# Kernel optimization log

Measured on AMD Instinct MI355X. Metric: run time of the kernel, lower is better.

Reference implementation:

```python
import jax, jax.numpy as jnp
import numpy as np

B, FIELDS, D = 4096, 100, 64
HEADS, HID = 4, 16  # concat dim = HEADS*HID = 64


def _pairs(fields):
    # enumerate_fields_fn: all (i, j) with i < j
    left, right = [], []
    for i in range(fields - 1):
        for j in range(i + 1, fields):
            left.append(i)
            right.append(j)
    return np.asarray(left, np.int32), np.asarray(right, np.int32)

LEFT, RIGHT = _pairs(FIELDS)  # each (P,) with P = FIELDS*(FIELDS-1)//2 = 4950


def setup_inputs() -> dict:
    key = jax.random.key(0)
    kx, kq, kk, kv = jax.random.split(key, 4)
    s = 1.0 / np.sqrt(D).astype(np.float32)  # xavier-ish scale
    return {
        "x": jax.random.normal(kx, (B, FIELDS, D), jnp.float32),
        "wq": jax.random.normal(kq, (D, HEADS * HID), jnp.float32) * s,
        "wk": jax.random.normal(kk, (D, HEADS * HID), jnp.float32) * s,
        "wv": jax.random.normal(kv, (D, HEADS * HID), jnp.float32) * s,
    }


def _mha(x, wq, wk, wv):
    # 'origin' multi-head attention: per-head scaled dot product, heads concatenated
    b, f, _ = x.shape
    q = (x @ wq).reshape(b, f, HEADS, HID)
    k = (x @ wk).reshape(b, f, HEADS, HID)
    v = (x @ wv).reshape(b, f, HEADS, HID)
    scores = jnp.einsum('bqhd,bkhd->bhqk', q, k) / jnp.sqrt(jnp.asarray(HID, x.dtype))
    attn = jax.nn.softmax(scores, axis=-1)            # (B, H, F, F)
    z = jnp.einsum('bhqk,bkhd->bqhd', attn, v)        # (B, F, H, HID)
    return z.reshape(b, f, HEADS * HID)


def reference(x, wq, wk, wv):
    # n_layers = 1, product_type = 'inner'
    z = _mha(x, wq, wk, wv)                           # (B, F, 64)
    # torch.gather(z, 1, index=(B,P,1)) -> picks channel 0 only (index shape == output shape)
    z_pol = z[:, LEFT, 0]                             # (B, P)
    x_pol = x[:, RIGHT, 0]                            # (B, P)
    p = z_pol * x_pol                                 # inner product then sum over last dim (size 1)
    # outputs = [sum(p, -1)]; cat along dim 0 of a single layer -> (B, P)
    return p
```

## Files before the change

kernel.cpp:

```cpp
#include <hip/hip_runtime.h>
#include <hip/hip_bf16.h>

namespace {
constexpr int F     = 100;
constexpr int D     = 64;
constexpr int HID   = 16;
constexpr int NPAIR = 4950;
constexpr int NT    = 256;
constexpr int SLD   = 101;
}

__global__ __launch_bounds__(NT, 2) void dcap_kernel(
    const float* __restrict__ x,
    const float* __restrict__ wq,
    const float* __restrict__ wk,
    const float* __restrict__ wv,
    float* __restrict__ out)
{
    __shared__ float sBuf[F * SLD];
    __shared__ float sQT[HID * F];
    __shared__ float sKT[HID * F];
    __shared__ float sWq[D * HID];
    __shared__ float sWk[D * HID];
    __shared__ float sWv[D];
    __shared__ float sV[F];
    __shared__ float sX0[F];
    __shared__ float sZ0[F];

    const int tid = threadIdx.x;
    const int b   = blockIdx.x;
    const float* __restrict__ xb = x + (size_t)b * (F * D);

    for (int i4 = tid; i4 < (F * D) / 4; i4 += NT) {
        const float4 v4 = reinterpret_cast<const float4*>(xb)[i4];
        const int g = i4 * 4;
        const int f = g >> 6;
        const int d = g & 63;
        sBuf[(d + 0) * F + f] = v4.x;
        sBuf[(d + 1) * F + f] = v4.y;
        sBuf[(d + 2) * F + f] = v4.z;
        sBuf[(d + 3) * F + f] = v4.w;
    }
    for (int i = tid; i < D * HID; i += NT) {
        const int d = i >> 4, h = i & 15;
        sWq[i] = wq[d * 64 + h];
        sWk[i] = wk[d * 64 + h];
    }
    if (tid < D) sWv[tid] = wv[tid * 64];
    __syncthreads();

    for (int t = tid; t < 200; t += NT) {
        const int isK = (t >= 100) ? 1 : 0;
        const int tt  = isK ? (t - 100) : t;
        const int f0  = (tt % 25) * 4;
        const int h0  = (tt / 25) * 4;
        const float* __restrict__ W  = isK ? sWk : sWq;
        float* __restrict__       OT = isK ? sKT : sQT;
        float acc[4][4] = {};
        #pragma unroll 8
        for (int d = 0; d < D; ++d) {
            const float4 xv  = *reinterpret_cast<const float4*>(&sBuf[d * F + f0]);
            const float4 wv4 = *reinterpret_cast<const float4*>(&W[d * HID + h0]);
            const float xa[4] = {xv.x, xv.y, xv.z, xv.w};
            const float wa[4] = {wv4.x, wv4.y, wv4.z, wv4.w};
            #pragma unroll
            for (int i = 0; i < 4; ++i)
                #pragma unroll
                for (int j = 0; j < 4; ++j)
                    acc[i][j] = fmaf(xa[i], wa[j], acc[i][j]);
        }
        #pragma unroll
        for (int j = 0; j < 4; ++j)
            #pragma unroll
            for (int i = 0; i < 4; ++i)
                OT[(h0 + j) * F + (f0 + i)] = acc[i][j];
    }
    if (tid < F) {
        float acc = 0.f;
        #pragma unroll 16
        for (int d = 0; d < D; ++d) acc = fmaf(sBuf[d * F + tid], sWv[d], acc);
        sV[tid]  = acc;
        sX0[tid] = sBuf[tid];
    }
    __syncthreads();

    for (int t = tid; t < 625; t += NT) {
        const int q0 = (t / 25) * 4;
        const int k0 = (t % 25) * 4;
        float acc[4][4] = {};
        #pragma unroll
        for (int d = 0; d < HID; ++d) {
            const float4 qv = *reinterpret_cast<const float4*>(&sQT[d * F + q0]);
            const float4 kv = *reinterpret_cast<const float4*>(&sKT[d * F + k0]);
            const float qa[4] = {qv.x, qv.y, qv.z, qv.w};
            const float ka[4] = {kv.x, kv.y, kv.z, kv.w};
            #pragma unroll
            for (int i = 0; i < 4; ++i)
                #pragma unroll
                for (int j = 0; j < 4; ++j)
                    acc[i][j] = fmaf(qa[i], ka[j], acc[i][j]);
        }
        #pragma unroll
        for (int i = 0; i < 4; ++i)
            #pragma unroll
            for (int j = 0; j < 4; ++j)
                sBuf[(q0 + i) * SLD + (k0 + j)] = acc[i][j] * 0.25f;
    }
    __syncthreads();

    if (tid < F) {
        const float* __restrict__ row = &sBuf[tid * SLD];
        float m = -1e30f;
        for (int k = 0; k < F; ++k) m = fmaxf(m, row[k]);
        float s = 0.f, a = 0.f;
        for (int k = 0; k < F; ++k) {
            const float e = __expf(row[k] - m);
            s += e;
            a = fmaf(e, sV[k], a);
        }
        sZ0[tid] = a / s;
    }
    __syncthreads();

    float* __restrict__ ob = out + (size_t)b * NPAIR;
    for (int i = tid; i < NPAIR; i += NT) {
        const float tf = sqrtf((float)(39601 - 8 * i));
        int l = (int)((199.0f - tf) * 0.5f);
        if (l < 0) l = 0;
        if (l > 98) l = 98;
        int base = (l * (199 - l)) >> 1;
        while (i < base) { --l; base = (l * (199 - l)) >> 1; }
        while (i >= base + (99 - l)) { base += (99 - l); ++l; }
        const int r = l + 1 + (i - base);
        ob[i] = sZ0[l] * sX0[r];
    }
}

extern "C" void kernel_launch(void* const* d_in, const int* in_sizes, int n_in,
                              void* d_out, int out_size, void* d_ws, size_t ws_size,
                              hipStream_t stream) {
    (void)in_sizes; (void)n_in; (void)out_size; (void)d_ws; (void)ws_size;
    const float* x  = (const float*)d_in[0];
    const float* wq = (const float*)d_in[1];
    const float* wk = (const float*)d_in[2];
    const float* wv = (const float*)d_in[3];
    float* out = (float*)d_out;
    dcap_kernel<<<dim3(4096), dim3(NT), 0, stream>>>(x, wq, wk, wv, out);
}
```

Measured before the change: 290.3 us.

## Fuse QK scores with softmax, project per-field rows from global memory

```diff
diff --git a/kernel.cpp b/kernel.cpp
--- a/kernel.cpp
+++ b/kernel.cpp
@@ -7,22 +7,21 @@
 constexpr int HID   = 16;
 constexpr int NPAIR = 4950;
 constexpr int NT    = 256;
-constexpr int SLD   = 101;
+constexpr int KLD   = 20;
 }
 
-__global__ __launch_bounds__(NT, 2) void dcap_kernel(
+__global__ __launch_bounds__(NT, 4) void dcap_kernel(
     const float* __restrict__ x,
     const float* __restrict__ wq,
     const float* __restrict__ wk,
     const float* __restrict__ wv,
     float* __restrict__ out)
 {
-    __shared__ float sBuf[F * SLD];
-    __shared__ float sQT[HID * F];
-    __shared__ float sKT[HID * F];
     __shared__ float sWq[D * HID];
     __shared__ float sWk[D * HID];
     __shared__ float sWv[D];
+    __shared__ float sQ[F * KLD];
+    __shared__ float sK[F * KLD];
     __shared__ float sV[F];
     __shared__ float sX0[F];
     __shared__ float sZ0[F];
@@ -31,16 +30,6 @@
     const int b   = blockIdx.x;
     const float* __restrict__ xb = x + (size_t)b * (F * D);
 
-    for (int i4 = tid; i4 < (F * D) / 4; i4 += NT) {
-        const float4 v4 = reinterpret_cast<const float4*>(xb)[i4];
-        const int g = i4 * 4;
-        const int f = g >> 6;
-        const int d = g & 63;
-        sBuf[(d + 0) * F + f] = v4.x;
-        sBuf[(d + 1) * F + f] = v4.y;
-        sBuf[(d + 2) * F + f] = v4.z;
-        sBuf[(d + 3) * F + f] = v4.w;
-    }
     for (int i = tid; i < D * HID; i += NT) {
         const int d = i >> 4, h = i & 15;
         sWq[i] = wq[d * 64 + h];
@@ -49,76 +38,103 @@
     if (tid < D) sWv[tid] = wv[tid * 64];
     __syncthreads();
 
-    for (int t = tid; t < 200; t += NT) {
-        const int isK = (t >= 100) ? 1 : 0;
-        const int tt  = isK ? (t - 100) : t;
-        const int f0  = (tt % 25) * 4;
-        const int h0  = (tt / 25) * 4;
-        const float* __restrict__ W  = isK ? sWk : sWq;
-        float* __restrict__       OT = isK ? sKT : sQT;
-        float acc[4][4] = {};
-        #pragma unroll 8
-        for (int d = 0; d < D; ++d) {
-            const float4 xv  = *reinterpret_cast<const float4*>(&sBuf[d * F + f0]);
-            const float4 wv4 = *reinterpret_cast<const float4*>(&W[d * HID + h0]);
+    if (tid < F) {
+        const int f = tid;
+        const float* __restrict__ xr = xb + f * D;
+        float q[HID] = {};
+        float v = 0.f;
+        for (int d4 = 0; d4 < D / 4; ++d4) {
+            const float4 xv = reinterpret_cast<const float4*>(xr)[d4];
             const float xa[4] = {xv.x, xv.y, xv.z, xv.w};
-            const float wa[4] = {wv4.x, wv4.y, wv4.z, wv4.w};
             #pragma unroll
-            for (int i = 0; i < 4; ++i)
-                #pragma unroll
-                for (int j = 0; j < 4; ++j)
-                    acc[i][j] = fmaf(xa[i], wa[j], acc[i][j]);
+            for (int j = 0; j < 4; ++j) {
+                const int d = d4 * 4 + j;
+                const float4 w0 = *reinterpret_cast<const float4*>(&sWq[d * HID + 0]);
+                const float4 w1 = *reinterpret_cast<const float4*>(&sWq[d * HID + 4]);
+                const float4 w2 = *reinterpret_cast<const float4*>(&sWq[d * HID + 8]);
+                const float4 w3 = *reinterpret_cast<const float4*>(&sWq[d * HID + 12]);
+                q[0]  = fmaf(xa[j], w0.x, q[0]);  q[1]  = fmaf(xa[j], w0.y, q[1]);
+                q[2]  = fmaf(xa[j], w0.z, q[2]);  q[3]  = fmaf(xa[j], w0.w, q[3]);
+                q[4]  = fmaf(xa[j], w1.x, q[4]);  q[5]  = fmaf(xa[j], w1.y, q[5]);
+                q[6]  = fmaf(xa[j], w1.z, q[6]);  q[7]  = fmaf(xa[j], w1.w, q[7]);
+                q[8]  = fmaf(xa[j], w2.x, q[8]);  q[9]  = fmaf(xa[j], w2.y, q[9]);
+                q[10] = fmaf(xa[j], w2.z, q[10]); q[11] = fmaf(xa[j], w2.w, q[11]);
+                q[12] = fmaf(xa[j], w3.x, q[12]); q[13] = fmaf(xa[j], w3.y, q[13]);
+                q[14] = fmaf(xa[j], w3.z, q[14]); q[15] = fmaf(xa[j], w3.w, q[15]);
+                v = fmaf(xa[j], sWv[d], v);
+            }
         }
         #pragma unroll
-        for (int j = 0; j < 4; ++j)
+        for (int h4 = 0; h4 < 4; ++h4)
+            *reinterpret_cast<float4*>(&sQ[f * KLD + h4 * 4]) =
+                make_float4(q[h4 * 4 + 0], q[h4 * 4 + 1], q[h4 * 4 + 2], q[h4 * 4 + 3]);
+        sV[f]  = v;
+        sX0[f] = xr[0];
+    } else if (tid >= 128 && tid < 128 + F) {
+        const int f = tid - 128;
+        const float* __restrict__ xr = xb + f * D;
+        float k[HID] = {};
+        for (int d4 = 0; d4 < D / 4; ++d4) {
+            const float4 xv = reinterpret_cast<const float4*>(xr)[d4];
+            const float xa[4] = {xv.x, xv.y, xv.z, xv.w};
             #pragma unroll
-            for (int i = 0; i < 4; ++i)
-                OT[(h0 + j) * F + (f0 + i)] = acc[i][j];
-    }
-    if (tid < F) {
-        float acc = 0.f;
-        #pragma unroll 16
-        for (int d = 0; d < D; ++d) acc = fmaf(sBuf[d * F + tid], sWv[d], acc);
-        sV[tid]  = acc;
-        sX0[tid] = sBuf[tid];
+            for (int j = 0; j < 4; ++j) {
+                const int d = d4 * 4 + j;
+                const float4 w0 = *reinterpret_cast<const float4*>(&sWk[d * HID + 0]);
+                const float4 w1 = *reinterpret_cast<const float4*>(&sWk[d * HID + 4]);
+                const float4 w2 = *reinterpret_cast<const float4*>(&sWk[d * HID + 8]);
+                const float4 w3 = *reinterpret_cast<const float4*>(&sWk[d * HID + 12]);
+                k[0]  = fmaf(xa[j], w0.x, k[0]);  k[1]  = fmaf(xa[j], w0.y, k[1]);
+                k[2]  = fmaf(xa[j], w0.z, k[2]);  k[3]  = fmaf(xa[j], w0.w, k[3]);
+                k[4]  = fmaf(xa[j], w1.x, k[4]);  k[5]  = fmaf(xa[j], w1.y, k[5]);
+                k[6]  = fmaf(xa[j], w1.z, k[6]);  k[7]  = fmaf(xa[j], w1.w, k[7]);
+                k[8]  = fmaf(xa[j], w2.x, k[8]);  k[9]  = fmaf(xa[j], w2.y, k[9]);
+                k[10] = fmaf(xa[j], w2.z, k[10]); k[11] = fmaf(xa[j], w2.w, k[11]);
+                k[12] = fmaf(xa[j], w3.x, k[12]); k[13] = fmaf(xa[j], w3.y, k[13]);
+                k[14] = fmaf(xa[j], w3.z, k[14]); k[15] = fmaf(xa[j], w3.w, k[15]);
+            }
+        }
+        #pragma unroll
+        for (int h4 = 0; h4 < 4; ++h4)
+            *reinterpret_cast<float4*>(&sK[f * KLD + h4 * 4]) =
+                make_float4(k[h4 * 4 + 0], k[h4 * 4 + 1], k[h4 * 4 + 2], k[h4 * 4 + 3]);
     }
     __syncthreads();
 
-    for (int t = tid; t < 625; t += NT) {
-        const int q0 = (t / 25) * 4;
-        const int k0 = (t % 25) * 4;
-        float acc[4][4] = {};
+    if (tid < 2 * F) {
+        const int r    = tid >> 1;
+        const int half = tid & 1;
+        float q[HID];
         #pragma unroll
-        for (int d = 0; d < HID; ++d) {
-            const float4 qv = *reinterpret_cast<const float4*>(&sQT[d * F + q0]);
-            const float4 kv = *reinterpret_cast<const float4*>(&sKT[d * F + k0]);
-            const float qa[4] = {qv.x, qv.y, qv.z, qv.w};
-            const float ka[4] = {kv.x, kv.y, kv.z, kv.w};
-            #pragma unroll
-            for (int i = 0; i < 4; ++i)
-                #pragma unroll
-                for (int j = 0; j < 4; ++j)
-                    acc[i][j] = fmaf(qa[i], ka[j], acc[i][j]);
+        for (int h4 = 0; h4 < 4; ++h4) {
+            const float4 t = *reinterpret_cast<const float4*>(&sQ[r * KLD + h4 * 4]);
+            q[h4 * 4 + 0] = t.x; q[h4 * 4 + 1] = t.y;
+            q[h4 * 4 + 2] = t.z; q[h4 * 4 + 3] = t.w;
         }
-        #pragma unroll
-        for (int i = 0; i < 4; ++i)
-            #pragma unroll
-            for (int j = 0; j < 4; ++j)
-                sBuf[(q0 + i) * SLD + (k0 + j)] = acc[i][j] * 0.25f;
-    }
-    __syncthreads();
-
-    if (tid < F) {
-        const float* __restrict__ row = &sBuf[tid * SLD];
-        float m = -1e30f;
-        for (int k = 0; k < F; ++k) m = fmaxf(m, row[k]);
-        float s = 0.f, a = 0.f;
-        for (int k = 0; k < F; ++k) {
-            const float e = __expf(row[k] - m);
+        float s = 0.f, z = 0.f;
+        const int k0 = half * 50;
+        for (int k = k0; k < k0 + 50; ++k) {
+            float d0 = 0.f, d1 = 0.f, d2 = 0.f, d3 = 0.f;
+            const float4 k0v = *reinterpret_cast<const float4*>(&sK[k * KLD + 0]);
+            const float4 k1v = *reinterpret_cast<const float4*>(&sK[k * KLD + 4]);
+            const float4 k2v = *reinterpret_cast<const float4*>(&sK[k * KLD + 8]);
+            const float4 k3v = *reinterpret_cast<const float4*>(&sK[k * KLD + 12]);
+            d0 = fmaf(q[0],  k0v.x, d0); d0 = fmaf(q[1],  k0v.y, d0);
+            d0 = fmaf(q[2],  k0v.z, d0); d0 = fmaf(q[3],  k0v.w, d0);
+            d1 = fmaf(q[4],  k1v.x, d1); d1 = fmaf(q[5],  k1v.y, d1);
+            d1 = fmaf(q[6],  k1v.z, d1); d1 = fmaf(q[7],  k1v.w, d1);
+            d2 = fmaf(q[8],  k2v.x, d2); d2 = fmaf(q[9],  k2v.y, d2);
+            d2 = fmaf(q[10], k2v.z, d2); d2 = fmaf(q[11], k2v.w, d2);
+            d3 = fmaf(q[12], k3v.x, d3); d3 = fmaf(q[13], k3v.y, d3);
+            d3 = fmaf(q[14], k3v.z, d3); d3 = fmaf(q[15], k3v.w, d3);
+            const float dot = (d0 + d1) + (d2 + d3);
+            const float e = __expf(dot * 0.25f);
             s += e;
-            a = fmaf(e, sV[k], a);
+            z = fmaf(e, sV[k], z);
         }
-        sZ0[tid] = a / s;
+        s += __shfl_xor(s, 1);
+        z += __shfl_xor(z, 1);
+        if (half == 0) sZ0[r] = z / s;
     }
     __syncthreads();
 
```

After: 237.8 us. -18.1%, faster.
